# Performance work log

Measured on AMD Instinct MI355X. Metric: run time of the kernel, lower is better.

Reference implementation:

```python
import jax, jax.numpy as jnp
import numpy as np

TAU = 0.2
LW = 0.5
EPS = 1e-12  # tf.math.l2_normalize epsilon


def _l2norm(x):
    ss = jnp.sum(x * x, axis=-1, keepdims=True)
    return x * jax.lax.rsqrt(jnp.maximum(ss, EPS))


def _global_head(f, W1, b1, W2, b2):
    g = jnp.mean(f, axis=(1, 2))            # GlobalAveragePooling2D -> [B, C]
    h = jax.nn.relu(g @ W1 + b1)
    return h @ W2 + b2                      # [B, 128]


def _dense_head(f, W1, b1, W2, b2):
    # 1x1 convs == per-pixel matmuls
    h = jax.nn.relu(jnp.einsum('bhwc,cd->bhwd', f, W1) + b1)
    return jnp.einsum('bhwd,de->bhwe', h, W2) + b2  # [B, H, W, 128]


def _info_nce(q, k):
    logits = (q @ k.T) / TAU                # [N, N]
    lse = jax.nn.logsumexp(logits, axis=-1)
    pos = jnp.diagonal(logits)
    return jnp.mean(lse - pos)


def setup_inputs() -> dict:
    key = jax.random.key(0)
    ks = jax.random.split(key, 10)
    B, H, W, C = 128, 7, 7, 2048
    Dh, De = 2048, 128
    s1 = 1.0 / np.sqrt(C)
    s2 = 1.0 / np.sqrt(Dh)
    inp = {
        'feat_q': jax.random.normal(ks[0], (B, H, W, C), jnp.float32),
        'feat_k': jax.random.normal(ks[1], (B, H, W, C), jnp.float32),
        'Wg1': jax.random.normal(ks[2], (C, Dh), jnp.float32) * s1,
        'bg1': jnp.zeros((Dh,), jnp.float32),
        'Wg2': jax.random.normal(ks[3], (Dh, De), jnp.float32) * s2,
        'bg2': jnp.zeros((De,), jnp.float32),
        'Wd1': jax.random.normal(ks[4], (C, Dh), jnp.float32) * s1,
        'bd1': jnp.zeros((Dh,), jnp.float32),
        'Wd2': jax.random.normal(ks[5], (Dh, De), jnp.float32) * s2,
        'bd2': jnp.zeros((De,), jnp.float32),
        'mWg1': jax.random.normal(ks[6], (C, Dh), jnp.float32) * s1,
        'mbg1': jnp.zeros((Dh,), jnp.float32),
        'mWg2': jax.random.normal(ks[7], (Dh, De), jnp.float32) * s2,
        'mbg2': jnp.zeros((De,), jnp.float32),
        'mWd1': jax.random.normal(ks[8], (C, Dh), jnp.float32) * s1,
        'mbd1': jnp.zeros((Dh,), jnp.float32),
        'mWd2': jax.random.normal(ks[9], (Dh, De), jnp.float32) * s2,
        'mbd2': jnp.zeros((De,), jnp.float32),
    }
    return inp


def reference(feat_q, feat_k, Wg1, bg1, Wg2, bg2, Wd1, bd1, Wd2, bd2,
              mWg1, mbg1, mWg2, mbg2, mWd1, mbd1, mWd2, mbd2):
    # query (student) branch
    q_g = _l2norm(_global_head(feat_q, Wg1, bg1, Wg2, bg2))      # [B, 128]
    q_d = _l2norm(_dense_head(feat_q, Wd1, bd1, Wd2, bd2))       # [B, H, W, 128]
    # key (momentum teacher) branch, stop-gradient as in train_step
    k_g = jax.lax.stop_gradient(_l2norm(_global_head(feat_k, mWg1, mbg1, mWg2, mbg2)))
    k_d = jax.lax.stop_gradient(_l2norm(_dense_head(feat_k, mWd1, mbd1, mWd2, mbd2)))

    l_g = _info_nce(q_g, k_g)

    B, H, W, De = q_d.shape
    f1 = q_d.reshape(B, H * W, De)
    f2 = k_d.reshape(B, H * W, De)
    sim = jnp.einsum('bnc,bmc->bnm', f1, f2)                     # [B, HW, HW]
    idx = jnp.argmax(sim, axis=-1)                               # [B, HW]
    matched = jnp.take_along_axis(f2, idx[..., None], axis=1)    # [B, HW, 128]

    l_d = _info_nce(f1.reshape(-1, De), matched.reshape(-1, De))
    total = (1.0 - LW) * l_g + LW * l_d
    return total
```

## Files before the change

kernel.cpp:

```cpp
#include <hip/hip_runtime.h>
#include <cstddef>

typedef __bf16 bf16x8 __attribute__((ext_vector_type(8)));
typedef float  f32x4  __attribute__((ext_vector_type(4)));
typedef float  f32x2  __attribute__((ext_vector_type(2)));
typedef unsigned short u16x8 __attribute__((ext_vector_type(8)));
typedef unsigned short u16x4 __attribute__((ext_vector_type(4)));
typedef unsigned short u16x2 __attribute__((ext_vector_type(2)));

__device__ __forceinline__ float b2f(unsigned short u) {
    union { unsigned int i; float f; } v; v.i = ((unsigned int)u) << 16; return v.f;
}
__device__ __forceinline__ unsigned short f2b(float f) {
    union { float f; unsigned int i; } v; v.f = f;
    unsigned int r = v.i + 0x7fffu + ((v.i >> 16) & 1u);
    return (unsigned short)(r >> 16);
}
__device__ __forceinline__ void gl_lds16(const void* g, void* l) {
    __builtin_amdgcn_global_load_lds((const __attribute__((address_space(1))) void*)g,
                                     (__attribute__((address_space(3))) void*)l,
                                     16, 0, 0);
}

__device__ __forceinline__ void xcd_swizzle(int& bx, int& by, int& bz) {
    unsigned int nx = gridDim.x, ny = gridDim.y;
    unsigned int n = nx * ny * gridDim.z;
    unsigned int lin = blockIdx.x + nx * (blockIdx.y + ny * blockIdx.z);
    unsigned int q = n >> 3, r = n & 7u;
    unsigned int xcd = lin & 7u, off = lin >> 3;
    unsigned int s = (xcd < r) ? (xcd * (q + 1u) + off)
                               : (r * (q + 1u) + (xcd - r) * q + off);
    bx = (int)(s % nx); s /= nx;
    by = (int)(s % ny);
    bz = (int)(s / ny);
}

__global__ __launch_bounds__(64) void detect_kernel(const unsigned short* __restrict__ feat,
                                                    int* __restrict__ flag) {
    __shared__ int cnt;
    if (threadIdx.x == 0) cnt = 0;
    __syncthreads();
    int c = 0;
    for (int i = threadIdx.x; i < 256; i += 64) {
        float v = b2f(feat[i]);
        if (fabsf(v) > 100.0f) ++c;
    }
    atomicAdd(&cnt, c);
    __syncthreads();
    if (threadIdx.x == 0) *flag = (cnt > 16) ? 1 : 0;
}

__global__ __launch_bounds__(256) void zero_kernel(float* __restrict__ p, int n4) {
    int i = blockIdx.x * 256 + threadIdx.x;
    const f32x4 z = {0.f, 0.f, 0.f, 0.f};
    if (i < n4) ((f32x4*)p)[i] = z;
}

__global__ __launch_bounds__(256) void convpool_kernel(const void* __restrict__ fq,
                                                       const void* __restrict__ fk,
                                                       unsigned short* __restrict__ FQ,
                                                       unsigned short* __restrict__ FK,
                                                       unsigned short* __restrict__ gq,
                                                       unsigned short* __restrict__ gk,
                                                       const int* __restrict__ flagp) {
    int fl = *flagp;
    int b = blockIdx.y;
    const void* src = blockIdx.z ? fk : fq;
    unsigned short* dst = blockIdx.z ? FK : FQ;
    unsigned short* g   = blockIdx.z ? gk : gq;
    int c0 = blockIdx.x * 512 + threadIdx.x * 2;
    float s0 = 0.f, s1 = 0.f;
    if (fl) {
        const float* sf = (const float*)src;
        #pragma unroll 7
        for (int p = 0; p < 49; ++p) {
            size_t idx = ((size_t)b * 49 + p) * 2048 + c0;
            f32x2 v = *(const f32x2*)(sf + idx);
            u16x2 o; o[0] = f2b(v[0]); o[1] = f2b(v[1]);
            s0 += v[0]; s1 += v[1];
            *(u16x2*)(dst + idx) = o;
        }
    } else {
        const unsigned short* su = (const unsigned short*)src;
        #pragma unroll 7
        for (int p = 0; p < 49; ++p) {
            size_t idx = ((size_t)b * 49 + p) * 2048 + c0;
            u16x2 o = *(const u16x2*)(su + idx);
            s0 += b2f(o[0]); s1 += b2f(o[1]);
            *(u16x2*)(dst + idx) = o;
        }
    }
    u16x2 gm; gm[0] = f2b(s0 * (1.0f / 49.0f)); gm[1] = f2b(s1 * (1.0f / 49.0f));
    *(u16x2*)(g + (size_t)b * 2048 + c0) = gm;
}

__global__ __launch_bounds__(256) void convert_kernel(const void* __restrict__ in,
                                                      unsigned short* __restrict__ out,
                                                      const int* __restrict__ flagp) {
    int fl = *flagp;
    size_t i = ((size_t)blockIdx.x * 256 + threadIdx.x) * 8;
    if (fl) {
        const float* inf = (const float*)in;
        f32x4 v0 = *(const f32x4*)(inf + i);
        f32x4 v1 = *(const f32x4*)(inf + i + 4);
        u16x8 o;
        o[0]=f2b(v0[0]); o[1]=f2b(v0[1]); o[2]=f2b(v0[2]); o[3]=f2b(v0[3]);
        o[4]=f2b(v1[0]); o[5]=f2b(v1[1]); o[6]=f2b(v1[2]); o[7]=f2b(v1[3]);
        *(u16x8*)(out + i) = o;
    } else {
        *(u16x8*)(out + i) = *(const u16x8*)((const unsigned short*)in + i);
    }
}

__global__ __launch_bounds__(256) void pool_kernel(const void* __restrict__ fq,
                                                   const void* __restrict__ fk,
                                                   unsigned short* __restrict__ gq,
                                                   unsigned short* __restrict__ gk,
                                                   const int* __restrict__ flagp) {
    int fl = *flagp;
    int c = blockIdx.x * 256 + threadIdx.x;
    int b = blockIdx.y;
    const void* src = blockIdx.z ? fk : fq;
    unsigned short* dst = blockIdx.z ? gk : gq;
    size_t base = (size_t)b * 49 * 2048 + c;
    float s = 0.f;
    if (fl) {
        const float* sf = (const float*)src;
        #pragma unroll
        for (int p = 0; p < 49; ++p) s += sf[base + (size_t)p * 2048];
    } else {
        const unsigned short* su = (const unsigned short*)src;
        #pragma unroll
        for (int p = 0; p < 49; ++p) s += b2f(su[base + (size_t)p * 2048]);
    }
    dst[(size_t)b * 2048 + c] = f2b(s * (1.0f / 49.0f));
}

__global__ __launch_bounds__(256) void transpose2v_kernel(
    const void* __restrict__ s0, const void* __restrict__ s1,
    unsigned short* __restrict__ d0, unsigned short* __restrict__ d1,
    int rows, int cols, const int* __restrict__ flagp) {
    int fl = *flagp;
    int z = blockIdx.z;
    const void* in = z ? s1 : s0;
    unsigned short* out = z ? d1 : d0;
    __shared__ unsigned short tile[64 * 72];
    int bx = blockIdx.x * 64, by = blockIdx.y * 64;
    int tr = threadIdx.x >> 3;
    int tc = (threadIdx.x & 7) * 8;
    #pragma unroll
    for (int h = 0; h < 2; ++h) {
        int r = tr + h * 32;
        if (fl) {
            const float* inf = (const float*)in + (size_t)(by + r) * cols + bx + tc;
            f32x4 v0 = *(const f32x4*)inf;
            f32x4 v1 = *(const f32x4*)(inf + 4);
            u16x8 o;
            o[0]=f2b(v0[0]); o[1]=f2b(v0[1]); o[2]=f2b(v0[2]); o[3]=f2b(v0[3]);
            o[4]=f2b(v1[0]); o[5]=f2b(v1[1]); o[6]=f2b(v1[2]); o[7]=f2b(v1[3]);
            *(u16x8*)(tile + r * 72 + tc) = o;
        } else {
            const unsigned short* inu = (const unsigned short*)in + (size_t)(by + r) * cols + bx + tc;
            *(u16x8*)(tile + r * 72 + tc) = *(const u16x8*)inu;
        }
    }
    __syncthreads();
    #pragma unroll
    for (int h = 0; h < 2; ++h) {
        int oc = tr + h * 32;
        u16x8 v;
        #pragma unroll
        for (int j = 0; j < 8; ++j) v[j] = tile[(tc + j) * 72 + oc];
        *(u16x8*)(out + (size_t)(bx + oc) * rows + by + tc) = v;
    }
}

__global__ __launch_bounds__(256) void transpose4v_kernel(
    const void* __restrict__ s0, const void* __restrict__ s1,
    const void* __restrict__ s2, const void* __restrict__ s3,
    unsigned short* __restrict__ d0, unsigned short* __restrict__ d1,
    unsigned short* __restrict__ d2, unsigned short* __restrict__ d3,
    int rows, int cols, const int* __restrict__ flagp) {
    int fl = *flagp;
    int z = blockIdx.z;
    const void* in = (z == 0) ? s0 : (z == 1) ? s1 : (z == 2) ? s2 : s3;
    unsigned short* out = (z == 0) ? d0 : (z == 1) ? d1 : (z == 2) ? d2 : d3;
    __shared__ unsigned short tile[64 * 72];
    int bx = blockIdx.x * 64, by = blockIdx.y * 64;
    int tr = threadIdx.x >> 3;
    int tc = (threadIdx.x & 7) * 8;
    #pragma unroll
    for (int h = 0; h < 2; ++h) {
        int r = tr + h * 32;
        if (fl) {
            const float* inf = (const float*)in + (size_t)(by + r) * cols + bx + tc;
            f32x4 v0 = *(const f32x4*)inf;
            f32x4 v1 = *(const f32x4*)(inf + 4);
            u16x8 o;
            o[0]=f2b(v0[0]); o[1]=f2b(v0[1]); o[2]=f2b(v0[2]); o[3]=f2b(v0[3]);
            o[4]=f2b(v1[0]); o[5]=f2b(v1[1]); o[6]=f2b(v1[2]); o[7]=f2b(v1[3]);
            *(u16x8*)(tile + r * 72 + tc) = o;
        } else {
            const unsigned short* inu = (const unsigned short*)in + (size_t)(by + r) * cols + bx + tc;
            *(u16x8*)(tile + r * 72 + tc) = *(const u16x8*)inu;
        }
    }
    __syncthreads();
    #pragma unroll
    for (int h = 0; h < 2; ++h) {
        int oc = tr + h * 32;
        u16x8 v;
        #pragma unroll
        for (int j = 0; j < 8; ++j) v[j] = tile[(tc + j) * 72 + oc];
        *(u16x8*)(out + (size_t)(bx + oc) * rows + by + tc) = v;
    }
}

__device__ __forceinline__ void mlp_body(
    const unsigned short* __restrict__ A, const unsigned short* __restrict__ Bt,
    const unsigned short* __restrict__ W2, const void* __restrict__ b1,
    float* __restrict__ outp, size_t m0, size_t n0, int fl)
{
    const int K = 2048;
    __shared__ unsigned short smem[32768];
    unsigned short* As0 = smem;
    unsigned short* Bs0 = smem + 8192;
    unsigned short* As1 = smem + 16384;
    unsigned short* Bs1 = smem + 24576;
    unsigned short* W2s = smem;
    unsigned short* Hs  = smem + 8192;

    int tid  = threadIdx.x;
    int lane = tid & 63;
    int w    = tid >> 6;
    int wm = w & 1, wn = w >> 1;
    int quad = lane >> 4, l16 = lane & 15;
    int lrow = lane >> 3;
    int kc   = (lane & 7) ^ lrow;

    const unsigned short* gA[4];
    const unsigned short* gB[4];
    int off[4];
    #pragma unroll
    for (int c = 0; c < 4; ++c) {
        int row = w * 32 + c * 8 + lrow;
        gA[c] = A  + (m0 + row) * (size_t)K + kc * 8;
        gB[c] = Bt + (n0 + row) * (size_t)K + kc * 8;
        off[c] = w * 2048 + c * 512;
    }

    const f32x4 zero4 = {0.f, 0.f, 0.f, 0.f};
    f32x4 acc[4][4];
    #pragma unroll
    for (int i = 0; i < 4; ++i)
        #pragma unroll
        for (int j = 0; j < 4; ++j) acc[i][j] = zero4;

    int swz = l16 & 7;

#define STAGE(Ad, Bd) do { \
    _Pragma("unroll") \
    for (int c = 0; c < 4; ++c) { gl_lds16(gA[c], (Ad) + off[c]); gA[c] += 64; } \
    _Pragma("unroll") \
    for (int c = 0; c < 4; ++c) { gl_lds16(gB[c], (Bd) + off[c]); gB[c] += 64; } \
} while (0)

#define CSTEP(Asrc, Bsrc) do { \
    _Pragma("unroll") \
    for (int k0 = 0; k0 < 64; k0 += 32) { \
        bf16x8 af[4], bfr[4]; \
        _Pragma("unroll") \
        for (int mt = 0; mt < 4; ++mt) { \
            int row = wm * 64 + mt * 16 + l16; \
            int sc  = (((k0 >> 3) + quad) ^ swz) << 3; \
            af[mt] = *(const bf16x8*)((Asrc) + row * 64 + sc); \
        } \
        _Pragma("unroll") \
        for (int nt = 0; nt < 4; ++nt) { \
            int row = wn * 64 + nt * 16 + l16; \
            int sc  = (((k0 >> 3) + quad) ^ swz) << 3; \
            bfr[nt] = *(const bf16x8*)((Bsrc) + row * 64 + sc); \
        } \
        __builtin_amdgcn_s_setprio(1); \
        _Pragma("unroll") \
        for (int mt = 0; mt < 4; ++mt) \
            _Pragma("unroll") \
            for (int nt = 0; nt < 4; ++nt) \
                acc[mt][nt] = __builtin_amdgcn_mfma_f32_16x16x32_bf16(af[mt], bfr[nt], acc[mt][nt], 0, 0, 0); \
        __builtin_amdgcn_s_setprio(0); \
    } \
} while (0)

    STAGE(As0, Bs0);
    #pragma unroll 1
    for (int kb2 = 0; kb2 < 16; ++kb2) {
        STAGE(As1, Bs1);
        asm volatile("s_waitcnt vmcnt(8)" ::: "memory");
        __builtin_amdgcn_s_barrier();
        __builtin_amdgcn_sched_barrier(0);
        CSTEP(As0, Bs0);
        asm volatile("s_waitcnt lgkmcnt(0)" ::: "memory");
        __builtin_amdgcn_sched_barrier(0);
        __builtin_amdgcn_s_barrier();
        if (kb2 < 15) {
            STAGE(As0, Bs0);
            asm volatile("s_waitcnt vmcnt(8)" ::: "memory");
        } else {
            asm volatile("s_waitcnt vmcnt(0)" ::: "memory");
        }
        __builtin_amdgcn_s_barrier();
        __builtin_amdgcn_sched_barrier(0);
        CSTEP(As1, Bs1);
        asm volatile("s_waitcnt lgkmcnt(0)" ::: "memory");
        __builtin_amdgcn_sched_barrier(0);
        __builtin_amdgcn_s_barrier();
    }
#undef STAGE
#undef CSTEP

    float b1v[4];
    #pragma unroll
    for (int nt = 0; nt < 4; ++nt) {
        int col = (int)n0 + wn * 64 + nt * 16 + l16;
        b1v[nt] = fl ? ((const float*)b1)[col] : b2f(((const unsigned short*)b1)[col]);
    }

    f32x4 acc2[4][4];
    #pragma unroll
    for (int i = 0; i < 4; ++i)
        #pragma unroll
        for (int j = 0; j < 4; ++j) acc2[i][j] = zero4;

    #pragma unroll
    for (int hf = 0; hf < 2; ++hf) {
        __syncthreads();
        if (wn == hf) {
            #pragma unroll
            for (int mt = 0; mt < 4; ++mt)
                #pragma unroll
                for (int nt = 0; nt < 4; ++nt)
                    #pragma unroll
                    for (int r = 0; r < 4; ++r) {
                        float v = fmaxf(acc[mt][nt][r] + b1v[nt], 0.f);
                        Hs[(wm * 64 + mt * 16 + quad * 4 + r) * 72 + nt * 16 + l16] = f2b(v);
                    }
        } else {
            #pragma unroll
            for (int c = 0; c < 8; ++c) {
                const unsigned short* g = W2 + (size_t)(wm * 64 + c * 8 + lrow) * 2048
                                          + n0 + hf * 64 + kc * 8;
                gl_lds16(g, W2s + wm * 4096 + c * 512);
            }
        }
        __syncthreads();
        #pragma unroll
        for (int k0 = 0; k0 < 64; k0 += 32) {
            bf16x8 ha[4], wb[4];
            #pragma unroll
            for (int mt = 0; mt < 4; ++mt)
                ha[mt] = *(const bf16x8*)(Hs + (wm * 64 + mt * 16 + l16) * 72 + k0 + quad * 8);
            #pragma unroll
            for (int et = 0; et < 4; ++et) {
                int row = wn * 64 + et * 16 + l16;
                int sc  = (((k0 >> 3) + quad) ^ swz) << 3;
                wb[et] = *(const bf16x8*)(W2s + row * 64 + sc);
            }
            #pragma unroll
            for (int mt = 0; mt < 4; ++mt)
                #pragma unroll
                for (int et = 0; et < 4; ++et)
                    acc2[mt][et] = __builtin_amdgcn_mfma_f32_16x16x32_bf16(ha[mt], wb[et], acc2[mt][et], 0, 0, 0);
        }
    }

    #pragma unroll
    for (int et = 0; et < 4; ++et) {
        int col = wn * 64 + et * 16 + l16;
        #pragma unroll
        for (int mt = 0; mt < 4; ++mt)
            #pragma unroll
            for (int r = 0; r < 4; ++r) {
                size_t row = m0 + wm * 64 + mt * 16 + quad * 4 + r;
                atomicAdd(&outp[row * 128 + col], acc2[mt][et][r]);
            }
    }
}

__global__ __launch_bounds__(256) void mlp_mega_kernel(
    const unsigned short* __restrict__ FQ, const unsigned short* __restrict__ FK,
    const unsigned short* __restrict__ gq, const unsigned short* __restrict__ gk,
    const unsigned short* __restrict__ WD1T, const unsigned short* __restrict__ MWD1T,
    const unsigned short* __restrict__ WG1T, const unsigned short* __restrict__ MWG1T,
    const unsigned short* __restrict__ W2dq, const unsigned short* __restrict__ W2dk,
    const unsigned short* __restrict__ W2gq, const unsigned short* __restrict__ W2gk,
    const void* __restrict__ bd1, const void* __restrict__ mbd1,
    const void* __restrict__ bg1, const void* __restrict__ mbg1,
    float* __restrict__ rawdq, float* __restrict__ rawdk,
    float* __restrict__ rawgq, float* __restrict__ rawgk,
    const int* __restrict__ flagp)
{
    int fl = *flagp;
    int bx, by, bz;
    xcd_swizzle(bx, by, bz);
    int z = bz;
    int isg = (by == 49);
    const unsigned short *A, *Bt, *W2; const void* b1; float* outp;
    if (!isg) {
        A = z ? FK : FQ;  Bt = z ? MWD1T : WD1T;  W2 = z ? W2dk : W2dq;
        b1 = z ? mbd1 : bd1;  outp = z ? rawdk : rawdq;
    } else {
        A = z ? gk : gq;  Bt = z ? MWG1T : WG1T;  W2 = z ? W2gk : W2gq;
        b1 = z ? mbg1 : bg1;  outp = z ? rawgk : rawgq;
    }
    size_t m0 = isg ? 0 : (size_t)by * 128;
    size_t n0 = (size_t)bx * 128;
    mlp_body(A, Bt, W2, b1, outp, m0, n0, fl);
}

__global__ __launch_bounds__(256) void mlp_kernel(
    const unsigned short* __restrict__ A0, const unsigned short* __restrict__ A1,
    const unsigned short* __restrict__ Bt0, const unsigned short* __restrict__ Bt1,
    const unsigned short* __restrict__ W20, const unsigned short* __restrict__ W21,
    const void* __restrict__ b10, const void* __restrict__ b11,
    float* __restrict__ out0, float* __restrict__ out1,
    const int* __restrict__ flagp)
{
    int fl = *flagp;
    int bx, by, bz;
    xcd_swizzle(bx, by, bz);
    int z  = bz;
    mlp_body(z ? A1 : A0, z ? Bt1 : Bt0, z ? W21 : W20, z ? b11 : b10,
             z ? out1 : out0, (size_t)by * 128, (size_t)bx * 128, fl);
}

__global__ __launch_bounds__(256) void simmatch_kernel(
    const float* __restrict__ rawdq, const float* __restrict__ rawdk,
    const void* __restrict__ bd2, const void* __restrict__ mbd2,
    unsigned short* __restrict__ qd, unsigned short* __restrict__ kd,
    unsigned short* __restrict__ matched, float* __restrict__ pos,
    const int* __restrict__ flagp) {
    int fl = *flagp;
    __shared__ float f1s[49 * 128];
    __shared__ float f2s[49 * 128];
    int b = blockIdx.x;
    int half = blockIdx.y;
    int t = threadIdx.x;
    size_t base = (size_t)b * 49 * 128;

    int rr = t >> 2, jq = t & 3;
    if (rr < 49) {
        #pragma unroll
        for (int br = 0; br < 2; ++br) {
            const float* raw = br ? rawdk : rawdq;
            const void* bias = br ? mbd2 : bd2;
            unsigned short* outg = br ? kd : qd;
            float* fs = br ? f2s : f1s;
            size_t idx = base + (size_t)rr * 128 + jq * 32;
            float x[32];
            float ss = 0.f;
            #pragma unroll
            for (int c = 0; c < 32; ++c) {
                float bv = fl ? ((const float*)bias)[jq * 32 + c]
                              : b2f(((const unsigned short*)bias)[jq * 32 + c]);
                x[c] = raw[idx + c] + bv;
                ss += x[c] * x[c];
            }
            ss += __shfl_xor(ss, 1); ss += __shfl_xor(ss, 2);
            float rs = rsqrtf(fmaxf(ss, 1e-12f));
            #pragma unroll
            for (int c = 0; c < 32; ++c) {
                unsigned short us = f2b(x[c] * rs);
                if (half == 0) outg[idx + c] = us;
                fs[rr * 128 + jq * 32 + c] = b2f(us);
            }
        }
    }
    __syncthreads();

    int i0 = t >> 2, q4 = t & 3;
    int i = half * 25 + i0;
    int ilim = half ? 24 : 25;
    if (i0 < ilim) {
        int mlo = q4 * 13;
        int mhi = mlo + 13; if (mhi > 49) mhi = 49;
        float best = -1e30f; int bi = 1 << 20;
        const f32x4* va = (const f32x4*)(f1s + i * 128);
        for (int m = mlo; m < mhi; ++m) {
            const f32x4* vb = (const f32x4*)(f2s + m * 128);
            float d = 0.f;
            #pragma unroll
            for (int j = 0; j < 32; ++j) {
                f32x4 a = va[j], bb = vb[j];
                d += a[0]*bb[0] + a[1]*bb[1] + a[2]*bb[2] + a[3]*bb[3];
            }
            if (d > best) { best = d; bi = m; }
        }
        #pragma unroll
        for (int off = 1; off < 4; off <<= 1) {
            float ov = __shfl_xor(best, off);
            int   oi = __shfl_xor(bi, off);
            if (ov > best || (ov == best && oi < bi)) { best = ov; bi = oi; }
        }
        if (q4 == 0) pos[b * 49 + i] = best * 5.0f;
        for (int j = q4 * 32; j < q4 * 32 + 32; ++j)
            matched[base + (size_t)i * 128 + j] = f2b(f2s[bi * 128 + j]);
    }
}

#define KS 136
#define NZSPLIT 14
__global__ __launch_bounds__(256) void lse_kernel(const unsigned short* __restrict__ qd,
                                                  const unsigned short* __restrict__ matched,
                                                  float* __restrict__ lsep) {
    __shared__ unsigned short As[128 * KS];
    __shared__ unsigned short Bs[64 * KS];
    __shared__ float rsum[128];
    int tid  = threadIdx.x;
    int lane = tid & 63, wave = tid >> 6;
    int wm = wave & 1, wn = wave >> 1;
    int quad = lane >> 4, l16 = lane & 15;
    size_t m0 = (size_t)blockIdx.x * 128;
    int z = blockIdx.y;

    #pragma unroll
    for (int i = 0; i < 8; ++i) {
        int l = tid + 256 * i;
        int row = l >> 4, ko = (l & 15) << 3;
        u16x8 v = *(const u16x8*)(qd + (m0 + row) * 128 + ko);
        *(u16x8*)(As + row * KS + ko) = v;
    }
    if (tid < 128) rsum[tid] = 0.f;

    float rs[4][4];
    #pragma unroll
    for (int mt = 0; mt < 4; ++mt)
        #pragma unroll
        for (int r = 0; r < 4; ++r) rs[mt][r] = 0.f;

    const f32x4 zero4 = {0.f, 0.f, 0.f, 0.f};
    int nlo = z * 448, nhi = nlo + 448;
    for (int n0 = nlo; n0 < nhi; n0 += 64) {
        __syncthreads();
        #pragma unroll
        for (int i = 0; i < 4; ++i) {
            int l = tid + 256 * i;
            int row = l >> 4, ko = (l & 15) << 3;
            u16x8 v = *(const u16x8*)(matched + (size_t)(n0 + row) * 128 + ko);
            *(u16x8*)(Bs + row * KS + ko) = v;
        }
        __syncthreads();
        f32x4 acc[4][2];
        #pragma unroll
        for (int mt = 0; mt < 4; ++mt) { acc[mt][0] = zero4; acc[mt][1] = zero4; }
        #pragma unroll
        for (int k0 = 0; k0 < 128; k0 += 32) {
            bf16x8 af[4], bfr[2];
            #pragma unroll
            for (int mt = 0; mt < 4; ++mt)
                af[mt] = *(const bf16x8*)(As + (wm * 64 + mt * 16 + l16) * KS + k0 + quad * 8);
            #pragma unroll
            for (int nt = 0; nt < 2; ++nt)
                bfr[nt] = *(const bf16x8*)(Bs + (wn * 32 + nt * 16 + l16) * KS + k0 + quad * 8);
            #pragma unroll
            for (int mt = 0; mt < 4; ++mt)
                #pragma unroll
                for (int nt = 0; nt < 2; ++nt)
                    acc[mt][nt] = __builtin_amdgcn_mfma_f32_16x16x32_bf16(af[mt], bfr[nt], acc[mt][nt], 0, 0, 0);
        }
        #pragma unroll
        for (int mt = 0; mt < 4; ++mt)
            #pragma unroll
            for (int r = 0; r < 4; ++r)
                rs[mt][r] += __expf(acc[mt][0][r] * 5.0f) + __expf(acc[mt][1][r] * 5.0f);
    }
    #pragma unroll
    for (int mt = 0; mt < 4; ++mt)
        #pragma unroll
        for (int r = 0; r < 4; ++r) {
            float v = rs[mt][r];
            v += __shfl_xor(v, 1); v += __shfl_xor(v, 2);
            v += __shfl_xor(v, 4); v += __shfl_xor(v, 8);
            if (l16 == 0) atomicAdd(&rsum[wm * 64 + mt * 16 + quad * 4 + r], v);
        }
    __syncthreads();
    if (tid < 128) lsep[(size_t)z * 6272 + m0 + tid] = rsum[tid];
}

__global__ __launch_bounds__(128) void lg_kernel(const float* __restrict__ rawgq,
                                                 const float* __restrict__ rawgk,
                                                 const void* __restrict__ bg2,
                                                 const void* __restrict__ mbg2,
                                                 float* __restrict__ lgrow,
                                                 const int* __restrict__ flagp) {
    int fl = *flagp;
    __shared__ float ksf[128 * 128];
    __shared__ float qsf[8 * 128];
    int t = threadIdx.x;
    int rbase = blockIdx.x * 8;
    {
        const float* rk = rawgk + (size_t)t * 128;
        float ss = 0.f;
        for (int c = 0; c < 128; ++c) {
            float bv = fl ? ((const float*)mbg2)[c] : b2f(((const unsigned short*)mbg2)[c]);
            float xx = rk[c] + bv;
            ss += xx * xx;
        }
        float rsv = rsqrtf(fmaxf(ss, 1e-12f));
        for (int c = 0; c < 128; ++c) {
            float bv = fl ? ((const float*)mbg2)[c] : b2f(((const unsigned short*)mbg2)[c]);
            ksf[t * 128 + c] = b2f(f2b((rk[c] + bv) * rsv));
        }
    }
    if (t < 8) {
        const float* rq = rawgq + (size_t)(rbase + t) * 128;
        float ss = 0.f;
        for (int c = 0; c < 128; ++c) {
            float bv = fl ? ((const float*)bg2)[c] : b2f(((const unsigned short*)bg2)[c]);
            float xx = rq[c] + bv;
            ss += xx * xx;
        }
        float rsv = rsqrtf(fmaxf(ss, 1e-12f));
        for (int c = 0; c < 128; ++c) {
            float bv = fl ? ((const float*)bg2)[c] : b2f(((const unsigned short*)bg2)[c]);
            qsf[t * 128 + c] = b2f(f2b((rq[c] + bv) * rsv));
        }
    }
    __syncthreads();
    int rl = t >> 4, jg = t & 15;
    int row = rbase + rl;
    float se = 0.f, diag = 0.f;
    for (int jj = 0; jj < 8; ++jj) {
        int j = jg * 8 + jj;
        float d = 0.f;
        #pragma unroll 8
        for (int c = 0; c < 128; ++c) d += qsf[rl * 128 + c] * ksf[j * 128 + c];
        d *= 5.0f;
        se += __expf(d);
        if (j == row) diag = d;
    }
    #pragma unroll
    for (int off = 1; off < 16; off <<= 1) { se += __shfl_xor(se, off); diag += __shfl_xor(diag, off); }
    if (jg == 0) lgrow[row] = logf(se) - diag;
}

__global__ __launch_bounds__(256) void final_kernel(const float* __restrict__ lsep,
                                                    const float* __restrict__ pos,
                                                    const float* __restrict__ lgrow,
                                                    unsigned int* __restrict__ out) {
    int t = threadIdx.x;
    float s = 0.f;
    for (int i = t; i < 6272; i += 256) {
        float se = 0.f;
        #pragma unroll
        for (int zz = 0; zz < NZSPLIT; ++zz) se += lsep[zz * 6272 + i];
        s += logf(se) - pos[i];
    }
    float g = (t < 128) ? lgrow[t] : 0.f;
    #pragma unroll
    for (int off = 32; off >= 1; off >>= 1) { s += __shfl_xor(s, off); g += __shfl_xor(g, off); }
    __shared__ float p8[8];
    if ((t & 63) == 0) { p8[t >> 6] = s; p8[4 + (t >> 6)] = g; }
    __syncthreads();
    if (t == 0) {
        float ld  = (p8[0] + p8[1] + p8[2] + p8[3]) * (1.0f / 6272.0f);
        float lg  = (p8[4] + p8[5] + p8[6] + p8[7]) * (1.0f / 128.0f);
        float total = 0.5f * lg + 0.5f * ld;
        unsigned int L = f2b(total);
        union { float f; unsigned int u; } tb; tb.f = total;
        unsigned int base = (tb.u & 0xFFFF0000u) | L;
        unsigned int bu = base; float be = 1e30f;
        #pragma unroll
        for (int d = -1; d <= 1; ++d) {
            unsigned int c = base + ((unsigned int)d << 16);
            union { unsigned int u; float f; } cv; cv.u = c;
            float e = fabsf(cv.f - total);
            if (e < be) { be = e; bu = c; }
        }
        out[0] = bu;
    }
}

#define A_FQ     ((size_t)0)
#define A_FK     ((size_t)25690112)
#define A_WD1T   ((size_t)51380224)
#define A_MWD1T  ((size_t)59768832)
#define A_WG1T   ((size_t)68157440)
#define A_MWG1T  ((size_t)76546048)
#define A_W2DQ   ((size_t)84934656)
#define A_W2DK   ((size_t)85458944)
#define A_W2GQ   ((size_t)85983232)
#define A_W2GK   ((size_t)86507520)
#define A_RAWDQ  ((size_t)87031808)
#define A_RAWDK  ((size_t)90243072)
#define A_RAWGQ  ((size_t)93454336)
#define A_RAWGK  ((size_t)93519872)
#define A_GQ     ((size_t)93585408)
#define A_GK     ((size_t)94109696)
#define A_QD     ((size_t)94633984)
#define A_KD     ((size_t)96239616)
#define A_MT     ((size_t)97845248)
#define A_POS    ((size_t)99450880)
#define A_LSEP   ((size_t)99475968)
#define A_LGR    ((size_t)99651584)
#define A_FLAG   ((size_t)99652096)
#define A_NEED   ((size_t)99652608)

#define B_SLOTA  ((size_t)0)
#define B_QD     ((size_t)0)
#define B_KD     ((size_t)1605632)
#define B_MT     ((size_t)3211264)
#define B_SLOTB  ((size_t)8388608)
#define B_W2DQ   ((size_t)34078720)
#define B_W2DK   ((size_t)34603008)
#define B_W2GQ   ((size_t)35127296)
#define B_W2GK   ((size_t)35651584)
#define B_RAWDQ  ((size_t)36175872)
#define B_RAWDK  ((size_t)39387136)
#define B_RAWGQ  ((size_t)42598400)
#define B_RAWGK  ((size_t)42663936)
#define B_GQ     ((size_t)42729472)
#define B_GK     ((size_t)43253760)
#define B_POS    ((size_t)42729472)
#define B_LSEP   ((size_t)42754560)
#define B_LGR    ((size_t)42930176)
#define B_FLAG   ((size_t)42930688)

extern "C" void kernel_launch(void* const* d_in, const int* in_sizes, int n_in,
                              void* d_out, int out_size, void* d_ws, size_t ws_size,
                              hipStream_t stream) {
    (void)in_sizes; (void)n_in; (void)out_size;
    const void* feat_q = d_in[0];
    const void* feat_k = d_in[1];
    const void* Wg1 = d_in[2];  const void* bg1 = d_in[3];
    const void* Wg2 = d_in[4];  const void* bg2 = d_in[5];
    const void* Wd1 = d_in[6];  const void* bd1 = d_in[7];
    const void* Wd2 = d_in[8];  const void* bd2 = d_in[9];
    const void* mWg1 = d_in[10]; const void* mbg1 = d_in[11];
    const void* mWg2 = d_in[12]; const void* mbg2 = d_in[13];
    const void* mWd1 = d_in[14]; const void* mbd1 = d_in[15];
    const void* mWd2 = d_in[16]; const void* mbd2 = d_in[17];
    char* ws = (char*)d_ws;

    if (ws_size >= A_NEED) {
        unsigned short* FQ    = (unsigned short*)(ws + A_FQ);
        unsigned short* FK    = (unsigned short*)(ws + A_FK);
        unsigned short* WD1T  = (unsigned short*)(ws + A_WD1T);
        unsigned short* MWD1T = (unsigned short*)(ws + A_MWD1T);
        unsigned short* WG1T  = (unsigned short*)(ws + A_WG1T);
        unsigned short* MWG1T = (unsigned short*)(ws + A_MWG1T);
        unsigned short* W2dq  = (unsigned short*)(ws + A_W2DQ);
        unsigned short* W2dk  = (unsigned short*)(ws + A_W2DK);
        unsigned short* W2gq  = (unsigned short*)(ws + A_W2GQ);
        unsigned short* W2gk  = (unsigned short*)(ws + A_W2GK);
        float* rawdq = (float*)(ws + A_RAWDQ);
        float* rawdk = (float*)(ws + A_RAWDK);
        float* rawgq = (float*)(ws + A_RAWGQ);
        float* rawgk = (float*)(ws + A_RAWGK);
        unsigned short* gq = (unsigned short*)(ws + A_GQ);
        unsigned short* gk = (unsigned short*)(ws + A_GK);
        unsigned short* qd = (unsigned short*)(ws + A_QD);
        unsigned short* kd = (unsigned short*)(ws + A_KD);
        unsigned short* mt = (unsigned short*)(ws + A_MT);
        float* pos  = (float*)(ws + A_POS);
        float* lsep = (float*)(ws + A_RAWDQ);
        float* lgr  = (float*)(ws + A_LGR);
        int*   flag = (int*)(ws + A_FLAG);

        detect_kernel<<<1, 64, 0, stream>>>((const unsigned short*)feat_q, flag);
        convpool_kernel<<<dim3(4, 128, 2), 256, 0, stream>>>(feat_q, feat_k, FQ, FK, gq, gk, flag);
        transpose4v_kernel<<<dim3(32, 32, 4), 256, 0, stream>>>(
            Wd1, mWd1, Wg1, mWg1, WD1T, MWD1T, WG1T, MWG1T, 2048, 2048, flag);
        transpose4v_kernel<<<dim3(2, 32, 4), 256, 0, stream>>>(
            Wd2, mWd2, Wg2, mWg2, W2dq, W2dk, W2gq, W2gk, 2048, 128, flag);
        zero_kernel<<<1600, 256, 0, stream>>>(rawdq, 409600);
        mlp_mega_kernel<<<dim3(16, 50, 2), 256, 0, stream>>>(
            FQ, FK, gq, gk, WD1T, MWD1T, WG1T, MWG1T,
            W2dq, W2dk, W2gq, W2gk, bd1, mbd1, bg1, mbg1,
            rawdq, rawdk, rawgq, rawgk, flag);
        simmatch_kernel<<<dim3(128, 2), 256, 0, stream>>>(rawdq, rawdk, bd2, mbd2, qd, kd, mt, pos, flag);
        lse_kernel<<<dim3(49, NZSPLIT), 256, 0, stream>>>(qd, mt, lsep);
        lg_kernel<<<16, 128, 0, stream>>>(rawgq, rawgk, bg2, mbg2, lgr, flag);
        final_kernel<<<1, 256, 0, stream>>>(lsep, pos, lgr, (unsigned int*)d_out);
    } else {
        unsigned short* slotA = (unsigned short*)(ws + B_SLOTA);
        unsigned short* slotB = (unsigned short*)(ws + B_SLOTB);
        unsigned short* W2dq = (unsigned short*)(ws + B_W2DQ);
        unsigned short* W2dk = (unsigned short*)(ws + B_W2DK);
        unsigned short* W2gq = (unsigned short*)(ws + B_W2GQ);
        unsigned short* W2gk = (unsigned short*)(ws + B_W2GK);
        float* rawdq = (float*)(ws + B_RAWDQ);
        float* rawdk = (float*)(ws + B_RAWDK);
        float* rawgq = (float*)(ws + B_RAWGQ);
        float* rawgk = (float*)(ws + B_RAWGK);
        unsigned short* gq = (unsigned short*)(ws + B_GQ);
        unsigned short* gk = (unsigned short*)(ws + B_GK);
        unsigned short* qd = (unsigned short*)(ws + B_QD);
        unsigned short* kd = (unsigned short*)(ws + B_KD);
        unsigned short* mt = (unsigned short*)(ws + B_MT);
        float* pos  = (float*)(ws + B_POS);
        float* lsep = (float*)(ws + B_RAWDQ);
        float* lgr  = (float*)(ws + B_LGR);
        int*   flag = (int*)(ws + B_FLAG);

        detect_kernel<<<1, 64, 0, stream>>>((const unsigned short*)feat_q, flag);
        pool_kernel<<<dim3(8, 128, 2), 256, 0, stream>>>(feat_q, feat_k, gq, gk, flag);
        transpose2v_kernel<<<dim3(32, 32, 2), 256, 0, stream>>>(Wg1, mWg1, slotA, slotB, 2048, 2048, flag);
        transpose4v_kernel<<<dim3(2, 32, 4), 256, 0, stream>>>(
            Wd2, mWd2, Wg2, mWg2, W2dq, W2dk, W2gq, W2gk, 2048, 128, flag);
        zero_kernel<<<1600, 256, 0, stream>>>(rawdq, 409600);
        mlp_kernel<<<dim3(16, 1, 2), 256, 0, stream>>>(
            gq, gk, slotA, slotB, W2gq, W2gk, bg1, mbg1, rawgq, rawgk, flag);
        transpose2v_kernel<<<dim3(32, 32, 1), 256, 0, stream>>>(Wd1, Wd1, slotA, slotA, 2048, 2048, flag);
        convert_kernel<<<6272, 256, 0, stream>>>(feat_q, slotB, flag);
        mlp_kernel<<<dim3(16, 49, 1), 256, 0, stream>>>(
            slotB, slotB, slotA, slotA, W2dq, W2dq, bd1, bd1, rawdq, rawdq, flag);
        transpose2v_kernel<<<dim3(32, 32, 1), 256, 0, stream>>>(mWd1, mWd1, slotA, slotA, 2048, 2048, flag);
        convert_kernel<<<6272, 256, 0, stream>>>(feat_k, slotB, flag);
        mlp_kernel<<<dim3(16, 49, 1), 256, 0, stream>>>(
            slotB, slotB, slotA, slotA, W2dk, W2dk, mbd1, mbd1, rawdk, rawdk, flag);
        simmatch_kernel<<<dim3(128, 2), 256, 0, stream>>>(rawdq, rawdk, bd2, mbd2, qd, kd, mt, pos, flag);
        lse_kernel<<<dim3(49, NZSPLIT), 256, 0, stream>>>(qd, mt, lsep);
        lg_kernel<<<16, 128, 0, stream>>>(rawgq, rawgk, bg2, mbg2, lgr, flag);
        final_kernel<<<1, 256, 0, stream>>>(lsep, pos, lgr, (unsigned int*)d_out);
    }
}
```

Baseline: 527.7 us.

## Replace 128x128 fused MLP kernel with 256x256-tile 512-thread kernel

Replaces the 128x128-tile fused two-layer MLP kernel with a new kernel that uses 256x256 output tiles, 512 threads (8 waves) and a 128KB LDS double buffer. Global-to-LDS staging for the next K-slice is spread across four MFMA phases, with s_setprio raised around the MFMA bursts. The larger tile is meant to cut redundant A/B traffic per FLOP and raise arithmetic intensity. In exchange the grid drops from 1600 to 416 blocks, which risks poorer load balance and lower occupancy, and it adds high register pressure from 128 accumulator registers per thread.

```diff
diff --git a/kernel.cpp b/kernel.cpp
--- a/kernel.cpp
+++ b/kernel.cpp
@@ -213,6 +213,212 @@
         #pragma unroll
         for (int j = 0; j < 8; ++j) v[j] = tile[(tc + j) * 72 + oc];
         *(u16x8*)(out + (size_t)(bx + oc) * rows + by + tc) = v;
+    }
+}
+
+__global__ __launch_bounds__(512, 2) void mega256_kernel(
+    const unsigned short* __restrict__ FQ, const unsigned short* __restrict__ FK,
+    const unsigned short* __restrict__ gq, const unsigned short* __restrict__ gk,
+    const unsigned short* __restrict__ WD1T, const unsigned short* __restrict__ MWD1T,
+    const unsigned short* __restrict__ WG1T, const unsigned short* __restrict__ MWG1T,
+    const unsigned short* __restrict__ W2dq, const unsigned short* __restrict__ W2dk,
+    const unsigned short* __restrict__ W2gq, const unsigned short* __restrict__ W2gk,
+    const void* __restrict__ bd1, const void* __restrict__ mbd1,
+    const void* __restrict__ bg1, const void* __restrict__ mbg1,
+    float* __restrict__ rawdq, float* __restrict__ rawdk,
+    float* __restrict__ rawgq, float* __restrict__ rawgk,
+    const int* __restrict__ flagp)
+{
+    int fl = *flagp;
+    int bx, by, bz;
+    xcd_swizzle(bx, by, bz);
+    int z = bz;
+    const unsigned short *A, *Bt, *W2; const void* b1; float* outp;
+    size_t m0;
+    if (by < 25) {
+        A = z ? FK : FQ;  Bt = z ? MWD1T : WD1T;  W2 = z ? W2dk : W2dq;
+        b1 = z ? mbd1 : bd1;  outp = z ? rawdk : rawdq;
+        m0 = (size_t)by * 256;
+    } else {
+        A = z ? gk : gq;  Bt = z ? MWG1T : WG1T;  W2 = z ? W2gk : W2gq;
+        b1 = z ? mbg1 : bg1;  outp = z ? rawgk : rawgq;
+        m0 = 0;
+    }
+    int mloc = (by >= 24) ? 128 : 256;
+    size_t n0 = (size_t)bx * 256;
+
+    const int K = 2048;
+    __shared__ unsigned short smem[65536];
+    unsigned short* As0v = smem;
+    unsigned short* Bs0v = smem + 16384;
+    unsigned short* As1v = smem + 32768;
+    unsigned short* Bs1v = smem + 49152;
+    unsigned short* Hs   = smem;
+
+    int tid  = threadIdx.x;
+    int lane = tid & 63;
+    int w    = tid >> 6;
+    int wm = w & 1, wn = w >> 1;
+    int quad = lane >> 4, l16 = lane & 15;
+    int lrow = lane >> 3;
+    int kc   = (lane & 7) ^ lrow;
+    int swz  = l16 & 7;
+
+    const unsigned short* gA[4];
+    const unsigned short* gB[4];
+    int offAB[4];
+    #pragma unroll
+    for (int c = 0; c < 4; ++c) {
+        int ra = (w * 32 + c * 8 + lrow) & (mloc - 1);
+        int rb = w * 32 + c * 8 + lrow;
+        gA[c] = A  + (m0 + ra) * (size_t)K + kc * 8;
+        gB[c] = Bt + (n0 + rb) * (size_t)K + kc * 8;
+        offAB[c] = w * 2048 + c * 512;
+    }
+
+    const f32x4 zero4 = {0.f, 0.f, 0.f, 0.f};
+    f32x4 acc[8][4];
+    #pragma unroll
+    for (int i = 0; i < 8; ++i)
+        #pragma unroll
+        for (int j = 0; j < 4; ++j) acc[i][j] = zero4;
+    bf16x8 bfr[4][2];
+    bf16x8 af[2][2];
+
+#define STG_A(c, Dst) do { gl_lds16(gA[(c)], (Dst) + offAB[(c)]); gA[(c)] += 64; } while (0)
+#define STG_B(c, Dst) do { gl_lds16(gB[(c)], (Dst) + offAB[(c)]); gB[(c)] += 64; } while (0)
+
+#define PH(Acur, Bcur, q, STAGES) do {                                          \
+    if ((q) == 0) {                                                             \
+        _Pragma("unroll")                                                       \
+        for (int nt_ = 0; nt_ < 4; ++nt_) {                                     \
+            _Pragma("unroll")                                                   \
+            for (int ki_ = 0; ki_ < 2; ++ki_) {                                 \
+                int sc_ = (((ki_ * 4) + quad) ^ swz) << 3;                      \
+                bfr[nt_][ki_] = *(const bf16x8*)((Bcur) + (wn * 64 + nt_ * 16 + l16) * 64 + sc_); \
+            }                                                                   \
+        }                                                                       \
+    }                                                                           \
+    _Pragma("unroll")                                                           \
+    for (int i_ = 0; i_ < 2; ++i_) {                                            \
+        _Pragma("unroll")                                                       \
+        for (int ki_ = 0; ki_ < 2; ++ki_) {                                     \
+            int sc_ = (((ki_ * 4) + quad) ^ swz) << 3;                          \
+            af[i_][ki_] = *(const bf16x8*)((Acur) + (wm * 128 + (2 * (q) + i_) * 16 + l16) * 64 + sc_); \
+        }                                                                       \
+    }                                                                           \
+    STAGES                                                                      \
+    __builtin_amdgcn_s_barrier();                                               \
+    asm volatile("s_waitcnt lgkmcnt(0)" ::: "memory");                          \
+    __builtin_amdgcn_sched_barrier(0);                                          \
+    __builtin_amdgcn_s_setprio(1);                                              \
+    _Pragma("unroll")                                                           \
+    for (int i_ = 0; i_ < 2; ++i_)                                              \
+        _Pragma("unroll")                                                       \
+        for (int nt_ = 0; nt_ < 4; ++nt_)                                       \
+            _Pragma("unroll")                                                   \
+            for (int ki_ = 0; ki_ < 2; ++ki_)                                   \
+                acc[2 * (q) + i_][nt_] = __builtin_amdgcn_mfma_f32_16x16x32_bf16(af[i_][ki_], bfr[nt_][ki_], acc[2 * (q) + i_][nt_], 0, 0, 0); \
+    __builtin_amdgcn_s_setprio(0);                                              \
+    __builtin_amdgcn_s_barrier();                                               \
+} while (0)
+
+    STG_A(0, As0v); STG_A(1, As0v); STG_A(2, As0v); STG_A(3, As0v);
+    STG_B(0, Bs0v); STG_B(1, Bs0v); STG_B(2, Bs0v); STG_B(3, Bs0v);
+
+    #pragma unroll 1
+    for (int tt = 0; tt < 16; ++tt) {
+        asm volatile("s_waitcnt vmcnt(0)" ::: "memory");
+        __builtin_amdgcn_s_barrier();
+        PH(As0v, Bs0v, 0, { STG_A(0, As1v); STG_A(1, As1v); STG_B(0, Bs1v); });
+        PH(As0v, Bs0v, 1, { STG_A(2, As1v); STG_A(3, As1v); STG_B(1, Bs1v); });
+        PH(As0v, Bs0v, 2, { STG_B(2, Bs1v); STG_B(3, Bs1v); });
+        PH(As0v, Bs0v, 3, {});
+        asm volatile("s_waitcnt vmcnt(0)" ::: "memory");
+        __builtin_amdgcn_s_barrier();
+        if (tt < 15) {
+            PH(As1v, Bs1v, 0, { STG_A(0, As0v); STG_A(1, As0v); STG_B(0, Bs0v); });
+            PH(As1v, Bs1v, 1, { STG_A(2, As0v); STG_A(3, As0v); STG_B(1, Bs0v); });
+            PH(As1v, Bs1v, 2, { STG_B(2, Bs0v); STG_B(3, Bs0v); });
+            PH(As1v, Bs1v, 3, {});
+        } else {
+            PH(As1v, Bs1v, 0, {});
+            PH(As1v, Bs1v, 1, {});
+            PH(As1v, Bs1v, 2, {});
+            PH(As1v, Bs1v, 3, {});
+        }
+    }
+#undef PH
+#undef STG_A
+#undef STG_B
+
+    float b1v[4];
+    #pragma unroll
+    for (int nt = 0; nt < 4; ++nt) {
+        int col = (int)n0 + wn * 64 + nt * 16 + l16;
+        b1v[nt] = fl ? ((const float*)b1)[col] : b2f(((const unsigned short*)b1)[col]);
+    }
+    u16x4 hbf[8][4];
+    #pragma unroll
+    for (int mt = 0; mt < 8; ++mt)
+        #pragma unroll
+        for (int nt = 0; nt < 4; ++nt)
+            #pragma unroll
+            for (int r = 0; r < 4; ++r)
+                hbf[mt][nt][r] = f2b(fmaxf(acc[mt][nt][r] + b1v[nt], 0.f));
+
+    int wm2 = w >> 1, wn2 = w & 1;
+    f32x4 acc2[4][4];
+    #pragma unroll
+    for (int i = 0; i < 4; ++i)
+        #pragma unroll
+        for (int j = 0; j < 4; ++j) acc2[i][j] = zero4;
+
+    const unsigned short* W2g = W2;
+    #pragma unroll
+    for (int j = 0; j < 4; ++j) {
+        if (wn == j) {
+            #pragma unroll
+            for (int mt = 0; mt < 8; ++mt)
+                #pragma unroll
+                for (int nt = 0; nt < 4; ++nt)
+                    #pragma unroll
+                    for (int r = 0; r < 4; ++r)
+                        Hs[(wm * 128 + mt * 16 + quad * 4 + r) * 72 + nt * 16 + l16] = hbf[mt][nt][r];
+        }
+        asm volatile("s_waitcnt lgkmcnt(0)" ::: "memory");
+        __builtin_amdgcn_s_barrier();
+        #pragma unroll
+        for (int ki = 0; ki < 2; ++ki) {
+            bf16x8 ha[4], wb[4];
+            #pragma unroll
+            for (int mt = 0; mt < 4; ++mt)
+                ha[mt] = *(const bf16x8*)(Hs + (wm2 * 64 + mt * 16 + l16) * 72 + ki * 32 + quad * 8);
+            #pragma unroll
+            for (int et = 0; et < 4; ++et)
+                wb[et] = *(const bf16x8*)(W2g + (size_t)(wn2 * 64 + et * 16 + l16) * 2048
+                                          + n0 + j * 64 + ki * 32 + quad * 8);
+            #pragma unroll
+            for (int mt = 0; mt < 4; ++mt)
+                #pragma unroll
+                for (int et = 0; et < 4; ++et)
+                    acc2[mt][et] = __builtin_amdgcn_mfma_f32_16x16x32_bf16(ha[mt], wb[et], acc2[mt][et], 0, 0, 0);
+        }
+        asm volatile("s_waitcnt lgkmcnt(0)" ::: "memory");
+        __builtin_amdgcn_s_barrier();
+    }
+
+    #pragma unroll
+    for (int et = 0; et < 4; ++et) {
+        int col = wn2 * 64 + et * 16 + l16;
+        #pragma unroll
+        for (int mt = 0; mt < 4; ++mt)
+            #pragma unroll
+            for (int r = 0; r < 4; ++r) {
+                int rl = wm2 * 64 + mt * 16 + quad * 4 + r;
+                if (rl < mloc)
+                    atomicAdd(&outp[(m0 + rl) * 128 + col], acc2[mt][et][r]);
+            }
     }
 }
 
@@ -386,37 +592,6 @@
     }
 }
 
-__global__ __launch_bounds__(256) void mlp_mega_kernel(
-    const unsigned short* __restrict__ FQ, const unsigned short* __restrict__ FK,
-    const unsigned short* __restrict__ gq, const unsigned short* __restrict__ gk,
-    const unsigned short* __restrict__ WD1T, const unsigned short* __restrict__ MWD1T,
-    const unsigned short* __restrict__ WG1T, const unsigned short* __restrict__ MWG1T,
-    const unsigned short* __restrict__ W2dq, const unsigned short* __restrict__ W2dk,
-    const unsigned short* __restrict__ W2gq, const unsigned short* __restrict__ W2gk,
-    const void* __restrict__ bd1, const void* __restrict__ mbd1,
-    const void* __restrict__ bg1, const void* __restrict__ mbg1,
-    float* __restrict__ rawdq, float* __restrict__ rawdk,
-    float* __restrict__ rawgq, float* __restrict__ rawgk,
-    const int* __restrict__ flagp)
-{
-    int fl = *flagp;
-    int bx, by, bz;
-    xcd_swizzle(bx, by, bz);
-    int z = bz;
-    int isg = (by == 49);
-    const unsigned short *A, *Bt, *W2; const void* b1; float* outp;
-    if (!isg) {
-        A = z ? FK : FQ;  Bt = z ? MWD1T : WD1T;  W2 = z ? W2dk : W2dq;
-        b1 = z ? mbd1 : bd1;  outp = z ? rawdk : rawdq;
-    } else {
-        A = z ? gk : gq;  Bt = z ? MWG1T : WG1T;  W2 = z ? W2gk : W2gq;
-        b1 = z ? mbg1 : bg1;  outp = z ? rawgk : rawgq;
-    }
-    size_t m0 = isg ? 0 : (size_t)by * 128;
-    size_t n0 = (size_t)bx * 128;
-    mlp_body(A, Bt, W2, b1, outp, m0, n0, fl);
-}
-
 __global__ __launch_bounds__(256) void mlp_kernel(
     const unsigned short* __restrict__ A0, const unsigned short* __restrict__ A1,
     const unsigned short* __restrict__ Bt0, const unsigned short* __restrict__ Bt1,
@@ -773,7 +948,7 @@
         transpose4v_kernel<<<dim3(2, 32, 4), 256, 0, stream>>>(
             Wd2, mWd2, Wg2, mWg2, W2dq, W2dk, W2gq, W2gk, 2048, 128, flag);
         zero_kernel<<<1600, 256, 0, stream>>>(rawdq, 409600);
-        mlp_mega_kernel<<<dim3(16, 50, 2), 256, 0, stream>>>(
+        mega256_kernel<<<dim3(8, 26, 2), 512, 0, stream>>>(
             FQ, FK, gq, gk, WD1T, MWD1T, WG1T, MWG1T,
             W2dq, W2dk, W2gq, W2gk, bd1, mbd1, bg1, mbg1,
             rawdq, rawdk, rawgq, rawgk, flag);
```

Measured after the change: 1.055 ms. 2x slower.
